# Optimization experiments

Measured on AMD Instinct MI355X. Metric: run time of the kernel, lower is better.

The kernel has to match this reference:

```python
import jax, jax.numpy as jnp
import numpy as np

Z = 128      # z_size
N = 256      # n_neurons_param_net
F = 2048     # n_functions
B = 8192     # batch


def setup_inputs() -> dict:
    key = jax.random.key(0)
    ks = jax.random.split(key, 16)
    sN = 1.0 / np.sqrt(N)
    inp = {
        "t": jax.random.uniform(ks[0], (1,), dtype=jnp.float32),
        "z_and_logpz": jax.random.normal(ks[1], (B, Z + 1), dtype=jnp.float32),
        # stacked first two layers of the 4 parameter-predicting MLPs
        # order: [w_in_net, w_out_net, b_net, gate_net]
        "W1": jax.random.normal(ks[2], (4, N, 1), dtype=jnp.float32),
        "B1": jax.random.normal(ks[3], (4, N), dtype=jnp.float32) * 0.01,
        "W2": jax.random.normal(ks[4], (4, N, N), dtype=jnp.float32) * sN,
        "B2": jax.random.normal(ks[5], (4, N), dtype=jnp.float32) * 0.01,
        # per-head final layers
        "W3_win": jax.random.normal(ks[6], (F * Z, N), dtype=jnp.float32) * sN,
        "b3_win": jax.random.normal(ks[7], (F * Z,), dtype=jnp.float32) * 0.01,
        "W3_wout": jax.random.normal(ks[8], (F * Z, N), dtype=jnp.float32) * sN,
        "b3_wout": jax.random.normal(ks[9], (F * Z,), dtype=jnp.float32) * 0.01,
        "W3_b": jax.random.normal(ks[10], (F, N), dtype=jnp.float32) * sN,
        "b3_b": jax.random.normal(ks[11], (F,), dtype=jnp.float32) * 0.01,
        "W3_gate": jax.random.normal(ks[12], (F, N), dtype=jnp.float32) * sN,
        "b3_gate": jax.random.normal(ks[13], (F,), dtype=jnp.float32) * 0.01,
    }
    return inp


def reference(t, z_and_logpz, W1, B1, W2, B2, W3_win, b3_win,
              W3_wout, b3_wout, W3_b, b3_b, W3_gate, b3_gate):
    F_ = W3_b.shape[0]
    Z_ = W3_win.shape[0] // F_
    ts = t.reshape(())  # scalar time

    # parameter-predicting MLPs (4 tiny 3-layer MLPs, first 2 layers stacked)
    h0 = jnp.tanh(W1[:, :, 0] * ts + B1)                    # [4, N]
    h1 = jnp.tanh(jnp.einsum('knm,km->kn', W2, h0) + B2)    # [4, N]
    w_in = (W3_win @ h1[0] + b3_win).reshape(F_, Z_)        # [F, Z]
    w_out = (W3_wout @ h1[1] + b3_wout).reshape(F_, Z_)     # [F, Z]
    b = W3_b @ h1[2] + b3_b                                 # [F]
    gate = jax.nn.sigmoid(W3_gate @ h1[3] + b3_gate)        # [F]

    z = z_and_logpz[:, :Z_]                                 # [B, Z]
    h = jnp.tanh(z @ w_in.T + b)                            # [B, F]
    g = h * gate                                            # gated hidden
    dz_dt = (g @ w_out) / F_                                # mean over functions -> [B, Z]

    # exact Jacobian trace (analytic; identical to autograd trace of this net):
    # d f_i / d z_i = mean_f gate_f * (1 - h_f^2) * w_out[f,i] * w_in[f,i]
    s = jnp.sum(w_in * w_out, axis=1)                       # [F]
    trace = ((1.0 - h * h) * gate) @ s / F_                 # [B]
    dlogpz_dt = -trace[:, None]                             # [B, 1]
    return jnp.concatenate([dz_dt, dlogpz_dt], axis=-1)     # [B, Z+1]
```

## Files before the change

kernel.cpp:

```cpp
#include <hip/hip_runtime.h>
#include <hip/hip_bf16.h>
#include <math.h>

typedef float f32x4 __attribute__((ext_vector_type(4)));
typedef float f32x4u __attribute__((ext_vector_type(4))) __attribute__((aligned(4)));
typedef short s16x8 __attribute__((ext_vector_type(8)));

__device__ __forceinline__ float wave_reduce64(float v) {
#pragma unroll
    for (int m = 32; m > 0; m >>= 1) v += __shfl_xor(v, m, 64);
    return v;
}

__device__ __forceinline__ unsigned short f32_to_bf16_rn(float x) {
    unsigned int u = __float_as_uint(x);
    unsigned int r = (u + 0x7fffu + ((u >> 16) & 1u)) >> 16;
    return (unsigned short)r;
}
__device__ __forceinline__ float bf16_to_f32(unsigned short h) {
    return __uint_as_float(((unsigned int)h) << 16);
}

__global__ __launch_bounds__(256) void kA(const float* __restrict__ t,
                                          const float* __restrict__ W1, const float* __restrict__ B1,
                                          const float* __restrict__ W2, const float* __restrict__ B2,
                                          float* __restrict__ h1) {
    const int tid = threadIdx.x;
    const int wave = (blockIdx.x << 2) + (tid >> 6);
    const int lane = tid & 63;
    const int k = wave >> 8, n = wave & 255;
    const float ts = t[0];
    const int m0 = lane << 2;
    f32x4 w1 = *(const f32x4*)(W1 + k * 256 + m0);
    f32x4 b1 = *(const f32x4*)(B1 + k * 256 + m0);
    f32x4 w2 = *(const f32x4*)(W2 + (size_t)(k * 256 + n) * 256 + m0);
    float p = 0.f;
    p += w2.x * tanhf(w1.x * ts + b1.x);
    p += w2.y * tanhf(w1.y * ts + b1.y);
    p += w2.z * tanhf(w1.z * ts + b1.z);
    p += w2.w * tanhf(w1.w * ts + b1.w);
    p = wave_reduce64(p);
    if (lane == 0) h1[k * 256 + n] = tanhf(p + B2[k * 256 + n]);
}

__global__ __launch_bounds__(256) void kB(const float* __restrict__ Wwin, const float* __restrict__ bwin,
                                          const float* __restrict__ Wwout, const float* __restrict__ bwout,
                                          const float* __restrict__ Wb, const float* __restrict__ bb,
                                          const float* __restrict__ Wg, const float* __restrict__ bg,
                                          const float* __restrict__ h1,
                                          float* __restrict__ w_in, float* __restrict__ w_out,
                                          unsigned short* __restrict__ w_in_hi, unsigned short* __restrict__ w_in_lo,
                                          unsigned short* __restrict__ w_out_t,
                                          float* __restrict__ b_arr, float* __restrict__ gate) {
    const int lane = threadIdx.x & 63;
    const int wave0 = (blockIdx.x << 2) + (threadIdx.x >> 6);
    const int nwaves = gridDim.x << 2;
    const int m0 = lane << 2;
    for (int r = wave0; r < 528384; r += nwaves) {
        const float* W;
        const float* bias;
        const float* hp;
        int idx, seg;
        if (r < 262144) { seg = 0; idx = r; W = Wwin; bias = bwin; hp = h1; }
        else if (r < 524288) { seg = 1; idx = r - 262144; W = Wwout; bias = bwout; hp = h1 + 256; }
        else if (r < 526336) { seg = 2; idx = r - 524288; W = Wb; bias = bb; hp = h1 + 512; }
        else { seg = 3; idx = r - 526336; W = Wg; bias = bg; hp = h1 + 768; }
        f32x4 wv = *(const f32x4*)(W + (size_t)idx * 256 + m0);
        f32x4 hv = *(const f32x4*)(hp + m0);
        float p = wv.x * hv.x + wv.y * hv.y + wv.z * hv.z + wv.w * hv.w;
        p = wave_reduce64(p);
        if (lane == 0) {
            float v = p + bias[idx];
            if (seg == 0) {
                w_in[idx] = v;
                unsigned short hi = f32_to_bf16_rn(v);
                w_in_hi[idx] = hi;
                w_in_lo[idx] = f32_to_bf16_rn(v - bf16_to_f32(hi));
            } else if (seg == 1) {
                w_out[idx] = v;
                w_out_t[(size_t)(idx & 127) * 2048 + (idx >> 7)] = f32_to_bf16_rn(v);
            } else if (seg == 2) {
                b_arr[idx] = v;
            } else {
                gate[idx] = 1.f / (1.f + __expf(-v));
            }
        }
    }
}

__global__ __launch_bounds__(256) void kC(const float* __restrict__ w_in, const float* __restrict__ w_out,
                                          float* __restrict__ s) {
    const int f = (blockIdx.x << 2) + (threadIdx.x >> 6);
    const int lane = threadIdx.x & 63;
    float2 a = *(const float2*)(w_in + (size_t)f * 128 + lane * 2);
    float2 b = *(const float2*)(w_out + (size_t)f * 128 + lane * 2);
    float p = a.x * b.x + a.y * b.y;
    p = wave_reduce64(p);
    if (lane == 0) s[f] = p;
}

__global__ __launch_bounds__(256) void kD(const float* __restrict__ zin,
                                          const unsigned short* __restrict__ w_in_hi,
                                          const unsigned short* __restrict__ w_in_lo,
                                          const unsigned short* __restrict__ w_out_t,
                                          const float* __restrict__ b_arr, const float* __restrict__ gate,
                                          const float* __restrict__ s, float* __restrict__ out) {
    __shared__ __attribute__((aligned(16))) unsigned short g_lds[4][16][72];
    __shared__ __attribute__((aligned(16))) float red[2][64][36];

    const int tid = threadIdx.x;
    const int w = tid >> 6, lane = tid & 63;
    const int q = lane >> 4, lm = lane & 15;
    const int rowtile = w & 1, fhalf = w >> 1;
    const int b0 = blockIdx.x * 32 + rowtile * 16;
    const int brow = b0 + lm;

    s16x8 zh[4], zl[4];
#pragma unroll
    for (int kt = 0; kt < 4; kt++) {
        const float* zp = zin + (size_t)brow * 129 + kt * 32 + q * 8;
        f32x4u z0 = *(const f32x4u*)(zp);
        f32x4u z1 = *(const f32x4u*)(zp + 4);
        float zv[8] = {z0.x, z0.y, z0.z, z0.w, z1.x, z1.y, z1.z, z1.w};
#pragma unroll
        for (int j = 0; j < 8; j++) {
            unsigned short hi = f32_to_bf16_rn(zv[j]);
            zh[kt][j] = (short)hi;
            zl[kt][j] = (short)f32_to_bf16_rn(zv[j] - bf16_to_f32(hi));
        }
    }

    f32x4 acc2[8];
#pragma unroll
    for (int ct = 0; ct < 8; ct++) acc2[ct] = (f32x4){0.f, 0.f, 0.f, 0.f};
    float tr[4] = {0.f, 0.f, 0.f, 0.f};

    for (int ch = 0; ch < 16; ch++) {
        const int f0 = fhalf * 1024 + ch * 64;
#pragma unroll
        for (int nt = 0; nt < 4; nt++) {
            const int fc = f0 + nt * 16 + lm;
            const unsigned short* ph = w_in_hi + (size_t)fc * 128;
            const unsigned short* pl = w_in_lo + (size_t)fc * 128;
            f32x4 acc1 = {0.f, 0.f, 0.f, 0.f};
#pragma unroll
            for (int kt = 0; kt < 4; kt++) {
                s16x8 bh = *(const s16x8*)(ph + kt * 32 + q * 8);
                s16x8 bl = *(const s16x8*)(pl + kt * 32 + q * 8);
                acc1 = __builtin_amdgcn_mfma_f32_16x16x32_bf16(zh[kt], bh, acc1, 0, 0, 0);
                acc1 = __builtin_amdgcn_mfma_f32_16x16x32_bf16(zh[kt], bl, acc1, 0, 0, 0);
                acc1 = __builtin_amdgcn_mfma_f32_16x16x32_bf16(zl[kt], bh, acc1, 0, 0, 0);
            }
            const float gv = gate[fc], bv = b_arr[fc], sv = s[fc];
#pragma unroll
            for (int i = 0; i < 4; i++) {
                float pre = acc1[i] + bv;
                float e = __expf(2.f * pre);
                float th = 1.f - 2.f * __builtin_amdgcn_rcpf(e + 1.f);
                float g = th * gv;
                tr[i] += (1.f - th * th) * gv * sv;
                g_lds[w][q * 4 + i][nt * 16 + lm] = f32_to_bf16_rn(g);
            }
        }
#pragma unroll
        for (int kt2 = 0; kt2 < 2; kt2++) {
            s16x8 af = *(const s16x8*)&g_lds[w][lm][kt2 * 32 + q * 8];
#pragma unroll
            for (int ct = 0; ct < 8; ct++) {
                s16x8 bf = *(const s16x8*)(w_out_t + (size_t)(ct * 16 + lm) * 2048 + f0 + kt2 * 32 + q * 8);
                acc2[ct] = __builtin_amdgcn_mfma_f32_16x16x32_bf16(af, bf, acc2[ct], 0, 0, 0);
            }
        }
    }

    if (fhalf == 1) {
#pragma unroll
        for (int ct = 0; ct < 8; ct++) *(f32x4*)&red[rowtile][lane][ct * 4] = acc2[ct];
        *(f32x4*)&red[rowtile][lane][32] = (f32x4){tr[0], tr[1], tr[2], tr[3]};
    }
    __syncthreads();
    if (fhalf == 0) {
#pragma unroll
        for (int ct = 0; ct < 8; ct++) {
            f32x4 o = *(const f32x4*)&red[rowtile][lane][ct * 4];
            acc2[ct].x += o.x; acc2[ct].y += o.y; acc2[ct].z += o.z; acc2[ct].w += o.w;
        }
        f32x4 to = *(const f32x4*)&red[rowtile][lane][32];
        tr[0] += to.x; tr[1] += to.y; tr[2] += to.z; tr[3] += to.w;

        const float inv = 1.f / 2048.f;
#pragma unroll
        for (int ct = 0; ct < 8; ct++)
#pragma unroll
            for (int i = 0; i < 4; i++)
                out[(size_t)(b0 + q * 4 + i) * 129 + ct * 16 + lm] = acc2[ct][i] * inv;
#pragma unroll
        for (int i = 0; i < 4; i++) {
            float t2 = tr[i];
            t2 += __shfl_xor(t2, 1, 64);
            t2 += __shfl_xor(t2, 2, 64);
            t2 += __shfl_xor(t2, 4, 64);
            t2 += __shfl_xor(t2, 8, 64);
            if (lm == 0) out[(size_t)(b0 + q * 4 + i) * 129 + 128] = -t2 * inv;
        }
    }
}

extern "C" void kernel_launch(void* const* d_in, const int* in_sizes, int n_in,
                              void* d_out, int out_size, void* d_ws, size_t ws_size,
                              hipStream_t stream) {
    const float* t     = (const float*)d_in[0];
    const float* z     = (const float*)d_in[1];
    const float* W1    = (const float*)d_in[2];
    const float* B1    = (const float*)d_in[3];
    const float* W2    = (const float*)d_in[4];
    const float* B2    = (const float*)d_in[5];
    const float* W3win = (const float*)d_in[6];
    const float* b3win = (const float*)d_in[7];
    const float* W3wo  = (const float*)d_in[8];
    const float* b3wo  = (const float*)d_in[9];
    const float* W3b   = (const float*)d_in[10];
    const float* b3b   = (const float*)d_in[11];
    const float* W3g   = (const float*)d_in[12];
    const float* b3g   = (const float*)d_in[13];
    float* out = (float*)d_out;

    float* h1    = (float*)d_ws;
    float* w_in  = h1 + 1024;
    float* w_out = w_in + 262144;
    float* b_arr = w_out + 262144;
    float* gate  = b_arr + 2048;
    float* s     = gate + 2048;
    unsigned short* w_in_hi = (unsigned short*)(s + 2048);
    unsigned short* w_in_lo = w_in_hi + 262144;
    unsigned short* w_out_t = w_in_lo + 262144;

    kA<<<256, 256, 0, stream>>>(t, W1, B1, W2, B2, h1);
    kB<<<2048, 256, 0, stream>>>(W3win, b3win, W3wo, b3wo, W3b, b3b, W3g, b3g, h1,
                                 w_in, w_out, w_in_hi, w_in_lo, w_out_t, b_arr, gate);
    kC<<<512, 256, 0, stream>>>(w_in, w_out, s);
    kD<<<256, 256, 0, stream>>>(z, w_in_hi, w_in_lo, w_out_t, b_arr, gate, s, out);
    (void)in_sizes; (void)n_in; (void)out_size; (void)ws_size;
}
```

Measured before the change: 632.8 us.

## Process four rows per wave in kB and split kD across four F-quarters

kB now has each wave compute four consecutive output rows, with the h1 vectors hoisted into registers and the shuffle reductions interleaved. This raises memory-level parallelism and amortises the reduction cost over the 512 MB weight stream. kD now gives each block 16 batch rows, with the four waves each covering a quarter of F and reducing through LDS, and it launches 512 blocks. That doubles the number of blocks available to fill the CUs, at the cost of more LDS reduction and each block re-reading all of the w_in/w_out weights for fewer rows.

```diff
diff --git a/kernel.cpp b/kernel.cpp
--- a/kernel.cpp
+++ b/kernel.cpp
@@ -56,33 +56,49 @@
     const int wave0 = (blockIdx.x << 2) + (threadIdx.x >> 6);
     const int nwaves = gridDim.x << 2;
     const int m0 = lane << 2;
-    for (int r = wave0; r < 528384; r += nwaves) {
-        const float* W;
-        const float* bias;
-        const float* hp;
-        int idx, seg;
-        if (r < 262144) { seg = 0; idx = r; W = Wwin; bias = bwin; hp = h1; }
-        else if (r < 524288) { seg = 1; idx = r - 262144; W = Wwout; bias = bwout; hp = h1 + 256; }
-        else if (r < 526336) { seg = 2; idx = r - 524288; W = Wb; bias = bb; hp = h1 + 512; }
-        else { seg = 3; idx = r - 526336; W = Wg; bias = bg; hp = h1 + 768; }
-        f32x4 wv = *(const f32x4*)(W + (size_t)idx * 256 + m0);
-        f32x4 hv = *(const f32x4*)(hp + m0);
-        float p = wv.x * hv.x + wv.y * hv.y + wv.z * hv.z + wv.w * hv.w;
-        p = wave_reduce64(p);
-        if (lane == 0) {
-            float v = p + bias[idx];
+    const f32x4 h_win  = *(const f32x4*)(h1 + m0);
+    const f32x4 h_wout = *(const f32x4*)(h1 + 256 + m0);
+    const f32x4 h_b    = *(const f32x4*)(h1 + 512 + m0);
+    const f32x4 h_g    = *(const f32x4*)(h1 + 768 + m0);
+    for (int g = wave0; g < 132096; g += nwaves) {
+        const int r = g << 2;
+        const float* W; const float* bias; f32x4 hv; int idx, seg;
+        if (r < 262144)      { seg = 0; idx = r;          W = Wwin;  bias = bwin;  hv = h_win; }
+        else if (r < 524288) { seg = 1; idx = r - 262144; W = Wwout; bias = bwout; hv = h_wout; }
+        else if (r < 526336) { seg = 2; idx = r - 524288; W = Wb;    bias = bb;    hv = h_b; }
+        else                 { seg = 3; idx = r - 526336; W = Wg;    bias = bg;    hv = h_g; }
+        const float* base = W + (size_t)idx * 256 + m0;
+        f32x4 w0 = *(const f32x4*)(base);
+        f32x4 w1 = *(const f32x4*)(base + 256);
+        f32x4 w2 = *(const f32x4*)(base + 512);
+        f32x4 w3 = *(const f32x4*)(base + 768);
+        float p0 = w0.x * hv.x + w0.y * hv.y + w0.z * hv.z + w0.w * hv.w;
+        float p1 = w1.x * hv.x + w1.y * hv.y + w1.z * hv.z + w1.w * hv.w;
+        float p2 = w2.x * hv.x + w2.y * hv.y + w2.z * hv.z + w2.w * hv.w;
+        float p3 = w3.x * hv.x + w3.y * hv.y + w3.z * hv.z + w3.w * hv.w;
+#pragma unroll
+        for (int m = 32; m > 0; m >>= 1) {
+            p0 += __shfl_xor(p0, m, 64);
+            p1 += __shfl_xor(p1, m, 64);
+            p2 += __shfl_xor(p2, m, 64);
+            p3 += __shfl_xor(p3, m, 64);
+        }
+        if (lane < 4) {
+            float v = (lane == 0) ? p0 : (lane == 1) ? p1 : (lane == 2) ? p2 : p3;
+            const int id2 = idx + lane;
+            v += bias[id2];
             if (seg == 0) {
-                w_in[idx] = v;
+                w_in[id2] = v;
                 unsigned short hi = f32_to_bf16_rn(v);
-                w_in_hi[idx] = hi;
-                w_in_lo[idx] = f32_to_bf16_rn(v - bf16_to_f32(hi));
+                w_in_hi[id2] = hi;
+                w_in_lo[id2] = f32_to_bf16_rn(v - bf16_to_f32(hi));
             } else if (seg == 1) {
-                w_out[idx] = v;
-                w_out_t[(size_t)(idx & 127) * 2048 + (idx >> 7)] = f32_to_bf16_rn(v);
+                w_out[id2] = v;
+                w_out_t[(size_t)(id2 & 127) * 2048 + (id2 >> 7)] = f32_to_bf16_rn(v);
             } else if (seg == 2) {
-                b_arr[idx] = v;
+                b_arr[id2] = v;
             } else {
-                gate[idx] = 1.f / (1.f + __expf(-v));
+                gate[id2] = 1.f / (1.f + __expf(-v));
             }
         }
     }
@@ -106,13 +122,12 @@
                                           const float* __restrict__ b_arr, const float* __restrict__ gate,
                                           const float* __restrict__ s, float* __restrict__ out) {
     __shared__ __attribute__((aligned(16))) unsigned short g_lds[4][16][72];
-    __shared__ __attribute__((aligned(16))) float red[2][64][36];
+    __shared__ __attribute__((aligned(16))) float red[3][64][36];
 
     const int tid = threadIdx.x;
     const int w = tid >> 6, lane = tid & 63;
     const int q = lane >> 4, lm = lane & 15;
-    const int rowtile = w & 1, fhalf = w >> 1;
-    const int b0 = blockIdx.x * 32 + rowtile * 16;
+    const int b0 = blockIdx.x * 16;
     const int brow = b0 + lm;
 
     s16x8 zh[4], zl[4];
@@ -135,8 +150,8 @@
     for (int ct = 0; ct < 8; ct++) acc2[ct] = (f32x4){0.f, 0.f, 0.f, 0.f};
     float tr[4] = {0.f, 0.f, 0.f, 0.f};
 
-    for (int ch = 0; ch < 16; ch++) {
-        const int f0 = fhalf * 1024 + ch * 64;
+    for (int ch = 0; ch < 8; ch++) {
+        const int f0 = w * 512 + ch * 64;
 #pragma unroll
         for (int nt = 0; nt < 4; nt++) {
             const int fc = f0 + nt * 16 + lm;
@@ -173,20 +188,23 @@
         }
     }
 
-    if (fhalf == 1) {
-#pragma unroll
-        for (int ct = 0; ct < 8; ct++) *(f32x4*)&red[rowtile][lane][ct * 4] = acc2[ct];
-        *(f32x4*)&red[rowtile][lane][32] = (f32x4){tr[0], tr[1], tr[2], tr[3]};
+    if (w != 0) {
+#pragma unroll
+        for (int ct = 0; ct < 8; ct++) *(f32x4*)&red[w - 1][lane][ct * 4] = acc2[ct];
+        *(f32x4*)&red[w - 1][lane][32] = (f32x4){tr[0], tr[1], tr[2], tr[3]};
     }
     __syncthreads();
-    if (fhalf == 0) {
-#pragma unroll
-        for (int ct = 0; ct < 8; ct++) {
-            f32x4 o = *(const f32x4*)&red[rowtile][lane][ct * 4];
-            acc2[ct].x += o.x; acc2[ct].y += o.y; acc2[ct].z += o.z; acc2[ct].w += o.w;
-        }
-        f32x4 to = *(const f32x4*)&red[rowtile][lane][32];
-        tr[0] += to.x; tr[1] += to.y; tr[2] += to.z; tr[3] += to.w;
+    if (w == 0) {
+#pragma unroll
+        for (int ww = 0; ww < 3; ww++) {
+#pragma unroll
+            for (int ct = 0; ct < 8; ct++) {
+                f32x4 o = *(const f32x4*)&red[ww][lane][ct * 4];
+                acc2[ct].x += o.x; acc2[ct].y += o.y; acc2[ct].z += o.z; acc2[ct].w += o.w;
+            }
+            f32x4 to = *(const f32x4*)&red[ww][lane][32];
+            tr[0] += to.x; tr[1] += to.y; tr[2] += to.z; tr[3] += to.w;
+        }
 
         const float inv = 1.f / 2048.f;
 #pragma unroll
@@ -239,6 +257,6 @@
     kB<<<2048, 256, 0, stream>>>(W3win, b3win, W3wo, b3wo, W3b, b3b, W3g, b3g, h1,
                                  w_in, w_out, w_in_hi, w_in_lo, w_out_t, b_arr, gate);
     kC<<<512, 256, 0, stream>>>(w_in, w_out, s);
-    kD<<<256, 256, 0, stream>>>(z, w_in_hi, w_in_lo, w_out_t, b_arr, gate, s, out);
+    kD<<<512, 256, 0, stream>>>(z, w_in_hi, w_in_lo, w_out_t, b_arr, gate, s, out);
     (void)in_sizes; (void)n_in; (void)out_size; (void)ws_size;
 }
```

Result: no change. 635.0 us (+0.4%).
